# Performance work log

Hardware: AMD Instinct MI355X
Metric: run time of the kernel (lower is better)

Reference implementation:

```python
import jax, jax.numpy as jnp
import numpy as np

# Model dims (match init_kwargs / input_specs)
B, L, D = 4, 1024, 512
CHI, S = 32, 4          # bond_dim, spatial_bond_dim
TRUNC_THR = 1e-4        # relative SVD truncation threshold
LN_EPS = 1e-6


def setup_inputs() -> dict:
    key = jax.random.key(0)
    ks = jax.random.split(key, 6)
    def dense(k, fi, fo):
        return jax.random.normal(k, (fi, fo), jnp.float32) / np.float32(np.sqrt(fi))
    return {
        "x": jax.random.normal(ks[0], (B, L, D), jnp.float32),
        "W_site": dense(ks[1], D, CHI * S * CHI),
        "b_site": jnp.zeros((CHI * S * CHI,), jnp.float32),
        "W_bridge": dense(ks[2], S * CHI, CHI),
        "b_bridge": jnp.zeros((CHI,), jnp.float32),
        "W_out": dense(ks[3], CHI, D),
        "b_out": jnp.zeros((D,), jnp.float32),
        "gamma": jnp.ones((D,), jnp.float32),
        "beta": jnp.zeros((D,), jnp.float32),
        "W_gate": dense(ks[4], D, D),
        "b_gate": jnp.zeros((D,), jnp.float32),
    }


def _mps_temporal_scan(x, site_weights):
    """Sequential O(L*chi^2) MPS scan with per-step SVD truncation.

    x: [B, L, D]; site_weights: [B, L, chi, s, chi].
    State h_t [B, chi] is the (normalized) left environment vector. Each step
    contracts the left vector (state + input injection from the first chi
    features, since initial_state is zeros) with the site tensor, truncates
    small singular values (relative threshold), and accumulates log-norms.
    Returns outputs [B, L, s*chi] and log_probs [B, L].
    """
    u_seq = jnp.transpose(x[:, :, :CHI], (1, 0, 2))            # [L, B, chi]
    A_seq = jnp.transpose(site_weights, (1, 0, 2, 3, 4))        # [L, B, chi, s, chi]

    def step(h, inp):
        A, u = inp                                              # [B,chi,s,chi], [B,chi]
        left = h + u                                            # input-driven left vector
        M = jnp.einsum('bl,blpr->bpr', left, A)                 # [B, s, chi]
        U, Sv, Vh = jnp.linalg.svd(M, full_matrices=False)      # Sv: [B, min(s,chi)]
        mask = (Sv >= TRUNC_THR * Sv[:, :1]).astype(M.dtype)    # relative truncation
        St = Sv * mask
        Mt = jnp.einsum('bik,bk,bkr->bir', U, St, Vh)           # truncated site matrix
        nrm = jnp.sqrt(jnp.sum(St * St, axis=-1) + 1e-12)       # Frobenius norm -> log prob
        v = jnp.sum(Mt, axis=1)                                 # contract physical index
        h_new = v / (jnp.linalg.norm(v, axis=-1, keepdims=True) + 1e-12)
        return h_new, (Mt.reshape(Mt.shape[0], -1), jnp.log(nrm))

    h0 = jnp.zeros((x.shape[0], CHI), x.dtype)                  # initial_state = zeros
    _, (outs, logp) = jax.lax.scan(step, h0, (A_seq, u_seq))
    return jnp.transpose(outs, (1, 0, 2)), jnp.transpose(logp, (1, 0))


def reference(x, W_site, b_site, W_bridge, b_bridge, W_out, b_out,
              gamma, beta, W_gate, b_gate):
    x = x.astype(jnp.float32)
    Bb, Ll = x.shape[0], x.shape[1]
    # site_tensor_proj: Dense(chi*s*chi) applied directly to inputs
    site_weights = (x @ W_site + b_site).reshape(Bb, Ll, CHI, S, CHI)
    outs, _logp = _mps_temporal_scan(x, site_weights)           # [B, L, s*chi]
    y = outs @ W_bridge + b_bridge                              # mps_bridge -> [B,L,chi]
    y = y @ W_out + b_out                                       # output_projection -> [B,L,D]
    # LayerNorm(eps=1e-6)
    mu = jnp.mean(y, axis=-1, keepdims=True)
    var = jnp.mean((y - mu) ** 2, axis=-1, keepdims=True)
    yn = (y - mu) * jax.lax.rsqrt(var + LN_EPS) * gamma + beta
    # gated residual
    gate = jax.nn.sigmoid(x @ W_gate + b_gate)
    return gate * yn + (1.0 - gate) * x
```

## Files before the change

### kernel.cpp

```cpp
#include <hip/hip_runtime.h>
#include <math.h>

#define B_   4
#define L_   1024
#define D_   512
#define CHI_ 32
#define S_   4
#define BT_  (B_ * L_)
#define NC_  2560
#define DPRE 8

__device__ __forceinline__ float readlane_f(float v, int l) {
    return __int_as_float(__builtin_amdgcn_readlane(__float_as_int(v), l));
}

__device__ __forceinline__ float bpermute_f(int byte_idx, float v) {
    return __int_as_float(__builtin_amdgcn_ds_bpermute(byte_idx, __float_as_int(v)));
}

template <int CTRL>
__device__ __forceinline__ float dpp_add(float x) {
    int y = __builtin_amdgcn_update_dpp(0, __float_as_int(x), CTRL, 0xf, 0xf, true);
    return x + __int_as_float(y);
}

__device__ __forceinline__ float reduce32_to_lane31(float x) {
    x = dpp_add<0x111>(x);
    x = dpp_add<0x112>(x);
    x = dpp_add<0x114>(x);
    x = dpp_add<0x118>(x);
    x = dpp_add<0x142>(x);
    return x;
}

__device__ __forceinline__ float octet_sum(float x) {
    x = dpp_add<0x111>(x);
    x = dpp_add<0x112>(x);
    x = dpp_add<0x114>(x);
    return x;
}

__global__ __launch_bounds__(256) void buildW_kernel(
    const float* __restrict__ Ws, const float* __restrict__ bs,
    const float* __restrict__ Wb, const float* __restrict__ Wg,
    const float* __restrict__ bg, float* __restrict__ Wcomb,
    float* __restrict__ biasC)
{
    const int tid = threadIdx.x;

    if (blockIdx.x == 512) {
        for (int f = tid; f < NC_; f += 256) {
            float acc;
            if (f < 1024) {
                const int q = f >> 8, rem = f & 255, i = rem >> 2, e = rem & 3;
                const int l = 4 * (i & 7) + e, r = (i >> 3) + 8 * q;
                const float* p = bs + l * 128 + r;
                acc = p[0] + p[32] + p[64] + p[96];
            } else if (f < 2048) {
                const int g = f - 1024, l = g >> 5, j = g & 31;
                acc = 0.f;
                for (int pr = 0; pr < 128; ++pr)
                    acc = fmaf(bs[l * 128 + pr], Wb[pr * 32 + j], acc);
            } else {
                acc = bg[f - 2048];
            }
            biasC[f] = acc;
        }
        return;
    }

    __shared__ float wsrow[4096];
    __shared__ float wbs[4096];

    const int d = blockIdx.x;
    #pragma unroll
    for (int i = 0; i < 16; ++i) {
        wsrow[i * 256 + tid] = Ws[(size_t)d * 4096 + i * 256 + tid];
        wbs[i * 256 + tid]   = Wb[i * 256 + tid];
    }
    __syncthreads();

    float* wrow = Wcomb + (size_t)d * NC_;

    #pragma unroll
    for (int ii = 0; ii < 4; ++ii) {
        const int f = ii * 256 + tid;
        const int q = f >> 8, rem = f & 255, i = rem >> 2, e = rem & 3;
        const int l = 4 * (i & 7) + e, r = (i >> 3) + 8 * q;
        const float* p = wsrow + l * 128 + r;
        wrow[f] = p[0] + p[32] + p[64] + p[96];
    }
    #pragma unroll
    for (int ii = 0; ii < 4; ++ii) {
        const int g = ii * 256 + tid;
        const int l = g >> 5, j = g & 31;
        float acc = 0.f;
        #pragma unroll 8
        for (int pr = 0; pr < 128; ++pr)
            acc = fmaf(wsrow[l * 128 + pr], wbs[pr * 32 + j], acc);
        wrow[1024 + g] = acc;
    }
    #pragma unroll
    for (int ii = 0; ii < 2; ++ii) {
        const int c = ii * 256 + tid;
        wrow[2048 + c] = Wg[(size_t)d * 512 + c];
    }
}

__global__ __launch_bounds__(256) void gemm_bias_kernel(
    const float* __restrict__ A, const float* __restrict__ Bm,
    const float* __restrict__ bias, float* __restrict__ C,
    int M, int N, int K)
{
    __shared__ float As[32][68];
    __shared__ float Bs[32][64];

    const int tid = threadIdx.x;
    const int tx = tid & 15;
    const int ty = tid >> 4;
    const int m0 = blockIdx.y * 64;
    const int n0 = blockIdx.x * 64;

    float c[4][4] = {};

    for (int k0 = 0; k0 < K; k0 += 32) {
        {
            const int o = tid * 8;
            const int m = o >> 5;
            const int k = o & 31;
            const float* ap = A + (size_t)(m0 + m) * K + k0 + k;
            const float4 a0 = *(const float4*)ap;
            const float4 a1 = *(const float4*)(ap + 4);
            As[k + 0][m] = a0.x; As[k + 1][m] = a0.y;
            As[k + 2][m] = a0.z; As[k + 3][m] = a0.w;
            As[k + 4][m] = a1.x; As[k + 5][m] = a1.y;
            As[k + 6][m] = a1.z; As[k + 7][m] = a1.w;
        }
        {
            const int o = tid * 8;
            const int k = o >> 6;
            const int n = o & 63;
            const float* bp = Bm + (size_t)(k0 + k) * N + n0 + n;
            *(float4*)&Bs[k][n]     = *(const float4*)bp;
            *(float4*)&Bs[k][n + 4] = *(const float4*)(bp + 4);
        }
        __syncthreads();

        #pragma unroll
        for (int kk = 0; kk < 32; ++kk) {
            const float4 av = *(const float4*)&As[kk][ty * 4];
            const float4 bv = *(const float4*)&Bs[kk][tx * 4];
            const float a[4] = {av.x, av.y, av.z, av.w};
            const float b[4] = {bv.x, bv.y, bv.z, bv.w};
            #pragma unroll
            for (int i = 0; i < 4; ++i)
                #pragma unroll
                for (int j = 0; j < 4; ++j)
                    c[i][j] = fmaf(a[i], b[j], c[i][j]);
        }
        __syncthreads();
    }

    const float4 bv = *(const float4*)&bias[n0 + tx * 4];
    #pragma unroll
    for (int i = 0; i < 4; ++i) {
        float4 outv;
        outv.x = c[i][0] + bv.x;
        outv.y = c[i][1] + bv.y;
        outv.z = c[i][2] + bv.z;
        outv.w = c[i][3] + bv.w;
        *(float4*)&C[(size_t)(m0 + ty * 4 + i) * N + n0 + tx * 4] = outv;
    }
}

__global__ __launch_bounds__(256) void cvec_kernel(
    const float* __restrict__ Cc, const float* __restrict__ x,
    float* __restrict__ cBuf)
{
    const int tid  = threadIdx.x;
    const int lane = tid & 63;
    const int bt   = blockIdx.x * 4 + (tid >> 6);

    const float* base = Cc + (size_t)bt * NC_ + 4 * lane;
    float4 a0 = *(const float4*)(base + 0);
    float4 a1 = *(const float4*)(base + 256);
    float4 a2 = *(const float4*)(base + 512);
    float4 a3 = *(const float4*)(base + 768);

    const float u = x[(size_t)bt * D_ + (lane & 31)];
    const int idx0 = 16 * (lane & 7);
    const float u0 = bpermute_f(idx0 + 0,  u);
    const float u1 = bpermute_f(idx0 + 4,  u);
    const float u2 = bpermute_f(idx0 + 8,  u);
    const float u3 = bpermute_f(idx0 + 12, u);

    float p0 = fmaf(u3, a0.w, fmaf(u2, a0.z, fmaf(u1, a0.y, u0 * a0.x)));
    float p1 = fmaf(u3, a1.w, fmaf(u2, a1.z, fmaf(u1, a1.y, u0 * a1.x)));
    float p2 = fmaf(u3, a2.w, fmaf(u2, a2.z, fmaf(u1, a2.y, u0 * a2.x)));
    float p3 = fmaf(u3, a3.w, fmaf(u2, a3.z, fmaf(u1, a3.y, u0 * a3.x)));

    p0 = octet_sum(p0); p1 = octet_sum(p1);
    p2 = octet_sum(p2); p3 = octet_sum(p3);

    if ((lane & 7) == 7) {
        const int k = lane >> 3;
        float* cp = cBuf + (size_t)bt * 32 + k;
        cp[0]  = p0;
        cp[8]  = p1;
        cp[16] = p2;
        cp[24] = p3;
    }
}

__global__ __launch_bounds__(64, 1) void scan_kernel(
    const float* __restrict__ Cc, const float* __restrict__ cBuf,
    float* __restrict__ wOut)
{
    const int b   = blockIdx.x;
    const int tid = threadIdx.x;

    const float* At = Cc + (size_t)b * L_ * NC_ + 4 * tid;
    const float* cb = cBuf + (size_t)b * L_ * 32 + (tid & 31);
    float*       wo = wOut + (size_t)b * L_ * 64 + tid;

    const int idx0 = 16 * (tid & 7);
    const int idxR = 32 * (tid & 7) + 28;
    const bool selA = (tid >> 3) & 1;
    const bool selB = (tid >> 4) & 1;

    float4 areg[DPRE][4];
    float  creg[DPRE];

    #pragma unroll
    for (int j = 0; j < DPRE; ++j) {
        const float* ap = At + (size_t)j * NC_;
        #pragma unroll
        for (int q = 0; q < 4; ++q) areg[j][q] = *(const float4*)(ap + 256 * q);
        creg[j] = cb[j * 32];
    }

    float w = 0.f;

    for (int t = 0; t < L_; t += DPRE) {
        #pragma unroll
        for (int j = 0; j < DPRE; ++j) {
            wo[(t + j) * 64] = w;

            float red = reduce32_to_lane31(w * w);

            const float wb0 = bpermute_f(idx0 + 0,  w);
            const float wb1 = bpermute_f(idx0 + 4,  w);
            const float wb2 = bpermute_f(idx0 + 8,  w);
            const float wb3 = bpermute_f(idx0 + 12, w);

            float p0, p1, p2, p3;
            {
                const float4 a0 = areg[j][0], a1 = areg[j][1];
                const float4 a2 = areg[j][2], a3 = areg[j][3];
                p0 = fmaf(wb3, a0.w, fmaf(wb2, a0.z, fmaf(wb1, a0.y, wb0 * a0.x)));
                p1 = fmaf(wb3, a1.w, fmaf(wb2, a1.z, fmaf(wb1, a1.y, wb0 * a1.x)));
                p2 = fmaf(wb3, a2.w, fmaf(wb2, a2.z, fmaf(wb1, a2.y, wb0 * a2.x)));
                p3 = fmaf(wb3, a3.w, fmaf(wb2, a3.z, fmaf(wb1, a3.y, wb0 * a3.x)));
            }

            p0 = octet_sum(p0);
            p1 = octet_sum(p1);
            p2 = octet_sum(p2);
            p3 = octet_sum(p3);

            const float m0 = bpermute_f(idxR, p0);
            const float m1 = bpermute_f(idxR, p1);
            const float m2 = bpermute_f(idxR, p2);
            const float m3 = bpermute_f(idxR, p3);
            const float t0 = selA ? m1 : m0;
            const float t1 = selA ? m3 : m2;
            const float m  = selB ? t1 : t0;

            const float n2 = readlane_f(red, 31);
            const float rn = rsqrtf(n2 + 1e-24f);
            w = fmaf(m, rn, creg[j]);

            int tn = t + j + DPRE;
            if (tn > L_ - 1) tn = L_ - 1;
            const float* ap = At + (size_t)tn * NC_;
            #pragma unroll
            for (int q = 0; q < 4; ++q) areg[j][q] = *(const float4*)(ap + 256 * q);
            creg[j] = cb[tn * 32];
        }
    }
}

__global__ __launch_bounds__(128) void phaseB_kernel(
    const float* __restrict__ Cc, const float* __restrict__ x,
    const float* __restrict__ wBuf, const float* __restrict__ bb,
    float* __restrict__ y1)
{
    __shared__ float lf[32];
    __shared__ float part[4][32];

    const int bt = blockIdx.x;
    const int tid = threadIdx.x;

    if (tid < 64) {
        const float wv = wBuf[(size_t)bt * 64 + tid];
        float red = reduce32_to_lane31(wv * wv);
        const float n2 = readlane_f(red, 31);
        const float rn = rsqrtf(n2 + 1e-24f);
        if (tid < 32)
            lf[tid] = fmaf(wv, rn, x[(size_t)bt * D_ + tid]);
    }
    __syncthreads();

    const int j = tid & 31, q = tid >> 5;
    const float* Gp = Cc + (size_t)bt * NC_ + 1024;
    float p = 0.f;
    #pragma unroll
    for (int i = 0; i < 8; ++i)
        p = fmaf(lf[8 * q + i], Gp[(8 * q + i) * 32 + j], p);
    part[q][j] = p;
    __syncthreads();

    if (tid < 32)
        y1[bt * 32 + tid] = part[0][tid] + part[1][tid] + part[2][tid]
                          + part[3][tid] + bb[tid];
}

__global__ __launch_bounds__(256) void epilogue_kernel(
    const float* __restrict__ x, const float* __restrict__ y1buf,
    const float* __restrict__ Wout, const float* __restrict__ bout,
    const float* __restrict__ gamma, const float* __restrict__ beta,
    const float* __restrict__ Cc, float* __restrict__ out)
{
    __shared__ float ys[32];
    __shared__ float red1[4], red2[4];

    const int bt = blockIdx.x;
    const int tid = threadIdx.x;

    if (tid < 32) ys[tid] = y1buf[bt * 32 + tid];
    __syncthreads();

    float yv[2];
    #pragma unroll
    for (int q = 0; q < 2; ++q) {
        const int d = tid + q * 256;
        float acc = bout[d];
        #pragma unroll
        for (int j = 0; j < 32; ++j)
            acc = fmaf(ys[j], Wout[j * D_ + d], acc);
        yv[q] = acc;
    }

    float s1 = yv[0] + yv[1];
    float s2 = yv[0] * yv[0] + yv[1] * yv[1];
    #pragma unroll
    for (int m = 1; m <= 32; m <<= 1) {
        s1 += __shfl_xor(s1, m);
        s2 += __shfl_xor(s2, m);
    }
    const int wid = tid >> 6;
    if ((tid & 63) == 0) { red1[wid] = s1; red2[wid] = s2; }
    __syncthreads();
    const float S1 = red1[0] + red1[1] + red1[2] + red1[3];
    const float S2 = red2[0] + red2[1] + red2[2] + red2[3];
    const float mu  = S1 * (1.f / (float)D_);
    const float var = S2 * (1.f / (float)D_) - mu * mu;
    const float rstd = rsqrtf(var + 1e-6f);

    #pragma unroll
    for (int q = 0; q < 2; ++q) {
        const int d = tid + q * 256;
        const size_t gi = (size_t)bt * D_ + d;
        const float yn = (yv[q] - mu) * rstd * gamma[d] + beta[d];
        const float z = Cc[(size_t)bt * NC_ + 2048 + d];
        const float g = 1.f / (1.f + expf(-z));
        const float xv = x[gi];
        out[gi] = g * yn + (1.f - g) * xv;
    }
}

extern "C" void kernel_launch(void* const* d_in, const int* in_sizes, int n_in,
                              void* d_out, int out_size, void* d_ws, size_t ws_size,
                              hipStream_t stream)
{
    const float* x        = (const float*)d_in[0];
    const float* W_site   = (const float*)d_in[1];
    const float* b_site   = (const float*)d_in[2];
    const float* W_bridge = (const float*)d_in[3];
    const float* b_bridge = (const float*)d_in[4];
    const float* W_out    = (const float*)d_in[5];
    const float* b_out    = (const float*)d_in[6];
    const float* gamma    = (const float*)d_in[7];
    const float* beta     = (const float*)d_in[8];
    const float* W_gate   = (const float*)d_in[9];
    const float* b_gate   = (const float*)d_in[10];
    float* out = (float*)d_out;

    float* ws = (float*)d_ws;
    float* Wcomb = ws;
    float* biasC = Wcomb + (size_t)512 * NC_;
    float* Cc    = biasC + NC_;
    float* cBuf  = Cc    + (size_t)BT_ * NC_;
    float* wBuf  = cBuf  + (size_t)BT_ * 32;
    float* y1    = wBuf  + (size_t)BT_ * 64;

    buildW_kernel<<<dim3(513), dim3(256), 0, stream>>>(
        W_site, b_site, W_bridge, W_gate, b_gate, Wcomb, biasC);

    gemm_bias_kernel<<<dim3(NC_ / 64, BT_ / 64), dim3(256), 0, stream>>>(
        x, Wcomb, biasC, Cc, BT_, NC_, D_);

    cvec_kernel<<<dim3(BT_ / 4), dim3(256), 0, stream>>>(Cc, x, cBuf);

    scan_kernel<<<dim3(B_), dim3(64), 0, stream>>>(Cc, cBuf, wBuf);

    phaseB_kernel<<<dim3(BT_), dim3(128), 0, stream>>>(
        Cc, x, wBuf, b_bridge, y1);

    epilogue_kernel<<<dim3(BT_), dim3(256), 0, stream>>>(
        x, y1, W_out, b_out, gamma, beta, Cc, out);
}
```

Measured before the change: 461.7 us.

## Restructure scan to stream site tensors via global_load_lds ring buffer

The sequential scan kernel now prefetches each step's 1024-float site tensor and c-vector directly into a 16-slot LDS ring buffer using global_load_lds, with explicit vmcnt waits, instead of holding 8 steps of prefetched data in registers. The state is redistributed so each lane holds four components, computes the norm with an octet butterfly (no 32-lane reduction plus readlane), and writes the already-normalized state via raw buffer stores. The phaseB kernel therefore just reads the normalized state instead of recomputing the norm. This shortens the per-step dependency chain on the latency-bound single-wave scan, but relies on hand-tuned waitcnt counts and inline asm, which are fragile.

```diff
diff --git a/kernel.cpp b/kernel.cpp
--- a/kernel.cpp
+++ b/kernel.cpp
@@ -9,10 +9,8 @@
 #define BT_  (B_ * L_)
 #define NC_  2560
 #define DPRE 8
-
-__device__ __forceinline__ float readlane_f(float v, int l) {
-    return __int_as_float(__builtin_amdgcn_readlane(__float_as_int(v), l));
-}
+#define SLOTS 16
+#define SLOT_F 1088
 
 __device__ __forceinline__ float bpermute_f(int byte_idx, float v) {
     return __int_as_float(__builtin_amdgcn_ds_bpermute(byte_idx, __float_as_int(v)));
@@ -22,15 +20,6 @@
 __device__ __forceinline__ float dpp_add(float x) {
     int y = __builtin_amdgcn_update_dpp(0, __float_as_int(x), CTRL, 0xf, 0xf, true);
     return x + __int_as_float(y);
-}
-
-__device__ __forceinline__ float reduce32_to_lane31(float x) {
-    x = dpp_add<0x111>(x);
-    x = dpp_add<0x112>(x);
-    x = dpp_add<0x114>(x);
-    x = dpp_add<0x118>(x);
-    x = dpp_add<0x142>(x);
-    return x;
 }
 
 __device__ __forceinline__ float octet_sum(float x) {
@@ -38,6 +27,35 @@
     x = dpp_add<0x112>(x);
     x = dpp_add<0x114>(x);
     return x;
+}
+
+__device__ __forceinline__ float octet_bfly(float x) {
+    x = dpp_add<0xB1>(x);
+    x = dpp_add<0x4E>(x);
+    x = dpp_add<0x141>(x);
+    return x;
+}
+
+typedef __attribute__((ext_vector_type(4))) unsigned int srd_t;
+
+__device__ __forceinline__ srd_t make_srd(const void* p, unsigned bytes) {
+    const unsigned long long a = (unsigned long long)p;
+    srd_t r;
+    r.x = (unsigned)a;
+    r.y = (unsigned)(a >> 32);
+    r.z = bytes;
+    r.w = 0x00020000u;
+    return r;
+}
+
+typedef __attribute__((address_space(1))) const void gas1_void;
+typedef __attribute__((address_space(3))) void las3_void;
+
+__device__ __forceinline__ void gl_lds16(const float* g, float* l) {
+    __builtin_amdgcn_global_load_lds((gas1_void*)g, (las3_void*)l, 16, 0, 0);
+}
+__device__ __forceinline__ void gl_lds4(const float* g, float* l) {
+    __builtin_amdgcn_global_load_lds((gas1_void*)g, (las3_void*)l, 4, 0, 0);
 }
 
 __global__ __launch_bounds__(256) void buildW_kernel(
@@ -212,87 +230,135 @@
     }
 }
 
+#define SCAN_STEP(TT, W)                                                        \
+    do {                                                                        \
+        const int t_is = (TT) + DPRE;                                           \
+        {                                                                       \
+            float* sl = ldsb + (t_is & (SLOTS - 1)) * SLOT_F;                   \
+            const float* ar = Abase + (size_t)t_is * NC_ + 4 * tid;             \
+            gl_lds16(ar,       sl);                                             \
+            gl_lds16(ar + 256, sl + 256);                                       \
+            gl_lds16(ar + 512, sl + 512);                                       \
+            gl_lds16(ar + 768, sl + 768);                                       \
+            gl_lds4(cbase + (size_t)t_is * 32 + tid, sl + 1024);                \
+        }                                                                       \
+        __builtin_amdgcn_sched_barrier(0);                                      \
+        asm volatile("s_waitcnt vmcnt(" W ")");                                 \
+        __builtin_amdgcn_sched_barrier(0);                                      \
+        const float* sr = ldsb + (((TT) + 1) & (SLOTS - 1)) * SLOT_F;           \
+        const float4 nA0 = *(const float4*)(sr + 4 * tid);                      \
+        const float4 nA1 = *(const float4*)(sr + 256 + 4 * tid);                \
+        const float4 nA2 = *(const float4*)(sr + 512 + 4 * tid);                \
+        const float4 nA3 = *(const float4*)(sr + 768 + 4 * tid);                \
+        const float4 nC  = *(const float4*)(sr + 1024 + 4 * h);                 \
+        float nn = fmaf(wb1, wb1, wb0 * wb0)                                    \
+                 + fmaf(wb3, wb3, wb2 * wb2);                                   \
+        nn = octet_bfly(nn);                                                    \
+        const float rn = rsqrtf(nn + 1e-24f);                                   \
+        float p0 = fmaf(wb1, cA0.y, wb0 * cA0.x)                                \
+                 + fmaf(wb3, cA0.w, wb2 * cA0.z);                               \
+        float p1 = fmaf(wb1, cA1.y, wb0 * cA1.x)                                \
+                 + fmaf(wb3, cA1.w, wb2 * cA1.z);                               \
+        float p2 = fmaf(wb1, cA2.y, wb0 * cA2.x)                                \
+                 + fmaf(wb3, cA2.w, wb2 * cA2.z);                               \
+        float p3 = fmaf(wb1, cA3.y, wb0 * cA3.x)                                \
+                 + fmaf(wb3, cA3.w, wb2 * cA3.z);                               \
+        p0 = octet_bfly(p0);                                                    \
+        p1 = octet_bfly(p1);                                                    \
+        p2 = octet_bfly(p2);                                                    \
+        p3 = octet_bfly(p3);                                                    \
+        const float rp = (tid & 2) ? ((tid & 1) ? p3 : p2)                      \
+                                   : ((tid & 1) ? p1 : p0);                     \
+        const float m0 = bpermute_f(idx0,      rp);                             \
+        const float m1 = bpermute_f(idx0 + 32, rp);                             \
+        const float m2 = bpermute_f(idx0 + 64, rp);                             \
+        const float m3 = bpermute_f(idx0 + 96, rp);                             \
+        const unsigned long long s01 =                                          \
+            ((unsigned long long)__float_as_uint(wb1 * rn) << 32) |             \
+            (unsigned)__float_as_uint(wb0 * rn);                                \
+        const unsigned long long s23 =                                          \
+            ((unsigned long long)__float_as_uint(wb3 * rn) << 32) |             \
+            (unsigned)__float_as_uint(wb2 * rn);                                \
+        asm volatile("buffer_store_dwordx2 %1, %0, %2, 0 offen"                 \
+                     :: "v"(voffW), "v"(s01), "s"(srdW));                       \
+        asm volatile("buffer_store_dwordx2 %1, %0, %2, 0 offen offset:8"        \
+                     :: "v"(voffW), "v"(s23), "s"(srdW));                       \
+        voffW += 128u;                                                          \
+        wb0 = fmaf(m0, rn, cC.x);                                               \
+        wb1 = fmaf(m1, rn, cC.y);                                               \
+        wb2 = fmaf(m2, rn, cC.z);                                               \
+        wb3 = fmaf(m3, rn, cC.w);                                               \
+        cA0 = nA0; cA1 = nA1; cA2 = nA2; cA3 = nA3; cC = nC;                    \
+        __builtin_amdgcn_sched_barrier(0);                                      \
+    } while (0)
+
 __global__ __launch_bounds__(64, 1) void scan_kernel(
     const float* __restrict__ Cc, const float* __restrict__ cBuf,
-    float* __restrict__ wOut)
-{
+    float* __restrict__ hnOut)
+{
+    __shared__ __align__(16) float ldsb[SLOTS * SLOT_F];
+
     const int b   = blockIdx.x;
     const int tid = threadIdx.x;
-
-    const float* At = Cc + (size_t)b * L_ * NC_ + 4 * tid;
-    const float* cb = cBuf + (size_t)b * L_ * 32 + (tid & 31);
-    float*       wo = wOut + (size_t)b * L_ * 64 + tid;
-
-    const int idx0 = 16 * (tid & 7);
-    const int idxR = 32 * (tid & 7) + 28;
-    const bool selA = (tid >> 3) & 1;
-    const bool selB = (tid >> 4) & 1;
-
-    float4 areg[DPRE][4];
-    float  creg[DPRE];
+    const int h   = tid & 7;
+
+    const float* Abase = Cc   + (size_t)b * L_ * NC_;
+    const float* cbase = cBuf + (size_t)b * L_ * 32;
+    const srd_t  srdW  = make_srd(hnOut + (size_t)b * L_ * 32,
+                                  (unsigned)(L_ * 32 * 4));
+
+    const int idx0 = 4 * (32 * (h & 1) + (h >> 1));
+
+    unsigned voffW = (unsigned)(h * 16);
 
     #pragma unroll
     for (int j = 0; j < DPRE; ++j) {
-        const float* ap = At + (size_t)j * NC_;
-        #pragma unroll
-        for (int q = 0; q < 4; ++q) areg[j][q] = *(const float4*)(ap + 256 * q);
-        creg[j] = cb[j * 32];
-    }
-
-    float w = 0.f;
-
-    for (int t = 0; t < L_; t += DPRE) {
-        #pragma unroll
-        for (int j = 0; j < DPRE; ++j) {
-            wo[(t + j) * 64] = w;
-
-            float red = reduce32_to_lane31(w * w);
-
-            const float wb0 = bpermute_f(idx0 + 0,  w);
-            const float wb1 = bpermute_f(idx0 + 4,  w);
-            const float wb2 = bpermute_f(idx0 + 8,  w);
-            const float wb3 = bpermute_f(idx0 + 12, w);
-
-            float p0, p1, p2, p3;
-            {
-                const float4 a0 = areg[j][0], a1 = areg[j][1];
-                const float4 a2 = areg[j][2], a3 = areg[j][3];
-                p0 = fmaf(wb3, a0.w, fmaf(wb2, a0.z, fmaf(wb1, a0.y, wb0 * a0.x)));
-                p1 = fmaf(wb3, a1.w, fmaf(wb2, a1.z, fmaf(wb1, a1.y, wb0 * a1.x)));
-                p2 = fmaf(wb3, a2.w, fmaf(wb2, a2.z, fmaf(wb1, a2.y, wb0 * a2.x)));
-                p3 = fmaf(wb3, a3.w, fmaf(wb2, a3.z, fmaf(wb1, a3.y, wb0 * a3.x)));
-            }
-
-            p0 = octet_sum(p0);
-            p1 = octet_sum(p1);
-            p2 = octet_sum(p2);
-            p3 = octet_sum(p3);
-
-            const float m0 = bpermute_f(idxR, p0);
-            const float m1 = bpermute_f(idxR, p1);
-            const float m2 = bpermute_f(idxR, p2);
-            const float m3 = bpermute_f(idxR, p3);
-            const float t0 = selA ? m1 : m0;
-            const float t1 = selA ? m3 : m2;
-            const float m  = selB ? t1 : t0;
-
-            const float n2 = readlane_f(red, 31);
-            const float rn = rsqrtf(n2 + 1e-24f);
-            w = fmaf(m, rn, creg[j]);
-
-            int tn = t + j + DPRE;
-            if (tn > L_ - 1) tn = L_ - 1;
-            const float* ap = At + (size_t)tn * NC_;
-            #pragma unroll
-            for (int q = 0; q < 4; ++q) areg[j][q] = *(const float4*)(ap + 256 * q);
-            creg[j] = cb[tn * 32];
-        }
-    }
-}
+        float* sl = ldsb + j * SLOT_F;
+        const float* ar = Abase + (size_t)j * NC_ + 4 * tid;
+        gl_lds16(ar,       sl);
+        gl_lds16(ar + 256, sl + 256);
+        gl_lds16(ar + 512, sl + 512);
+        gl_lds16(ar + 768, sl + 768);
+        gl_lds4(cbase + (size_t)j * 32 + tid, sl + 1024);
+    }
+    __builtin_amdgcn_sched_barrier(0);
+    asm volatile("s_waitcnt vmcnt(35)");
+    __builtin_amdgcn_sched_barrier(0);
+
+    float4 cA0 = *(const float4*)(ldsb + 4 * tid);
+    float4 cA1 = *(const float4*)(ldsb + 256 + 4 * tid);
+    float4 cA2 = *(const float4*)(ldsb + 512 + 4 * tid);
+    float4 cA3 = *(const float4*)(ldsb + 768 + 4 * tid);
+    float4 cC  = *(const float4*)(ldsb + 1024 + 4 * h);
+
+    float wb0 = 0.f, wb1 = 0.f, wb2 = 0.f, wb3 = 0.f;
+
+    SCAN_STEP(0, "35");
+    SCAN_STEP(1, "37");
+    SCAN_STEP(2, "39");
+    SCAN_STEP(3, "41");
+    SCAN_STEP(4, "43");
+    SCAN_STEP(5, "45");
+    SCAN_STEP(6, "47");
+    SCAN_STEP(7, "49");
+
+    for (int t = DPRE; t < L_; t += DPRE) {
+        SCAN_STEP(t + 0, "49");
+        SCAN_STEP(t + 1, "49");
+        SCAN_STEP(t + 2, "49");
+        SCAN_STEP(t + 3, "49");
+        SCAN_STEP(t + 4, "49");
+        SCAN_STEP(t + 5, "49");
+        SCAN_STEP(t + 6, "49");
+        SCAN_STEP(t + 7, "49");
+    }
+    asm volatile("s_waitcnt vmcnt(0)");
+}
+#undef SCAN_STEP
 
 __global__ __launch_bounds__(128) void phaseB_kernel(
     const float* __restrict__ Cc, const float* __restrict__ x,
-    const float* __restrict__ wBuf, const float* __restrict__ bb,
+    const float* __restrict__ hnBuf, const float* __restrict__ bb,
     float* __restrict__ y1)
 {
     __shared__ float lf[32];
@@ -301,14 +367,8 @@
     const int bt = blockIdx.x;
     const int tid = threadIdx.x;
 
-    if (tid < 64) {
-        const float wv = wBuf[(size_t)bt * 64 + tid];
-        float red = reduce32_to_lane31(wv * wv);
-        const float n2 = readlane_f(red, 31);
-        const float rn = rsqrtf(n2 + 1e-24f);
-        if (tid < 32)
-            lf[tid] = fmaf(wv, rn, x[(size_t)bt * D_ + tid]);
-    }
+    if (tid < 32)
+        lf[tid] = hnBuf[(size_t)bt * 32 + tid] + x[(size_t)bt * D_ + tid];
     __syncthreads();
 
     const int j = tid & 31, q = tid >> 5;
@@ -401,8 +461,8 @@
     float* biasC = Wcomb + (size_t)512 * NC_;
     float* Cc    = biasC + NC_;
     float* cBuf  = Cc    + (size_t)BT_ * NC_;
-    float* wBuf  = cBuf  + (size_t)BT_ * 32;
-    float* y1    = wBuf  + (size_t)BT_ * 64;
+    float* hnBuf = cBuf  + (size_t)BT_ * 32;
+    float* y1    = hnBuf + (size_t)BT_ * 32;
 
     buildW_kernel<<<dim3(513), dim3(256), 0, stream>>>(
         W_site, b_site, W_bridge, W_gate, b_gate, Wcomb, biasC);
@@ -412,10 +472,10 @@
 
     cvec_kernel<<<dim3(BT_ / 4), dim3(256), 0, stream>>>(Cc, x, cBuf);
 
-    scan_kernel<<<dim3(B_), dim3(64), 0, stream>>>(Cc, cBuf, wBuf);
+    scan_kernel<<<dim3(B_), dim3(64), 0, stream>>>(Cc, cBuf, hnBuf);
 
     phaseB_kernel<<<dim3(BT_), dim3(128), 0, stream>>>(
-        Cc, x, wBuf, b_bridge, y1);
+        Cc, x, hnBuf, b_bridge, y1);
 
     epilogue_kernel<<<dim3(BT_), dim3(256), 0, stream>>>(
         x, y1, W_out, b_out, gamma, beta, Cc, out);
```

Result: slower. 642.0 us (+39.1%).

## Enlarge GEMM tile to 128x128 with 8x8 register micro-tiles per thread

Applied to the files above, without the earlier changes.

The fp32 GEMM that produces the combined site/bridge/gate projections now uses 128x128 block tiles, with each thread computing an 8x8 register tile instead of 4x4. This doubles arithmetic per shared-memory load and cuts global reloads of A and B tiles. In exchange it raises register pressure and leaves only 20x32=640 blocks, which could lower occupancy on a 256-CU device.

```diff
diff --git a/kernel.cpp b/kernel.cpp
--- a/kernel.cpp
+++ b/kernel.cpp
@@ -112,34 +112,32 @@
     const float* __restrict__ bias, float* __restrict__ C,
     int M, int N, int K)
 {
-    __shared__ float As[32][68];
-    __shared__ float Bs[32][64];
+    __shared__ float As[32][132];
+    __shared__ float Bs[32][132];
 
     const int tid = threadIdx.x;
     const int tx = tid & 15;
     const int ty = tid >> 4;
-    const int m0 = blockIdx.y * 64;
-    const int n0 = blockIdx.x * 64;
-
-    float c[4][4] = {};
+    const int m0 = blockIdx.y * 128;
+    const int n0 = blockIdx.x * 128;
+
+    float acc[8][8] = {};
 
     for (int k0 = 0; k0 < K; k0 += 32) {
-        {
-            const int o = tid * 8;
-            const int m = o >> 5;
-            const int k = o & 31;
-            const float* ap = A + (size_t)(m0 + m) * K + k0 + k;
-            const float4 a0 = *(const float4*)ap;
-            const float4 a1 = *(const float4*)(ap + 4);
-            As[k + 0][m] = a0.x; As[k + 1][m] = a0.y;
-            As[k + 2][m] = a0.z; As[k + 3][m] = a0.w;
-            As[k + 4][m] = a1.x; As[k + 5][m] = a1.y;
-            As[k + 6][m] = a1.z; As[k + 7][m] = a1.w;
+        #pragma unroll
+        for (int p = 0; p < 4; ++p) {
+            const int m = (tid >> 3) + 32 * p;
+            const int k = (tid & 7) * 4;
+            const float4 av = *(const float4*)(A + (size_t)(m0 + m) * K + k0 + k);
+            As[k + 0][m] = av.x;
+            As[k + 1][m] = av.y;
+            As[k + 2][m] = av.z;
+            As[k + 3][m] = av.w;
         }
-        {
-            const int o = tid * 8;
-            const int k = o >> 6;
-            const int n = o & 63;
+        #pragma unroll
+        for (int p = 0; p < 2; ++p) {
+            const int k = (tid >> 4) + 16 * p;
+            const int n = (tid & 15) * 8;
             const float* bp = Bm + (size_t)(k0 + k) * N + n0 + n;
             *(float4*)&Bs[k][n]     = *(const float4*)bp;
             *(float4*)&Bs[k][n + 4] = *(const float4*)(bp + 4);
@@ -148,28 +146,33 @@
 
         #pragma unroll
         for (int kk = 0; kk < 32; ++kk) {
-            const float4 av = *(const float4*)&As[kk][ty * 4];
-            const float4 bv = *(const float4*)&Bs[kk][tx * 4];
-            const float a[4] = {av.x, av.y, av.z, av.w};
-            const float b[4] = {bv.x, bv.y, bv.z, bv.w};
+            const float4 a0 = *(const float4*)&As[kk][ty * 8];
+            const float4 a1 = *(const float4*)&As[kk][ty * 8 + 4];
+            const float4 b0 = *(const float4*)&Bs[kk][tx * 8];
+            const float4 b1 = *(const float4*)&Bs[kk][tx * 8 + 4];
+            const float a[8] = {a0.x, a0.y, a0.z, a0.w, a1.x, a1.y, a1.z, a1.w};
+            const float b[8] = {b0.x, b0.y, b0.z, b0.w, b1.x, b1.y, b1.z, b1.w};
             #pragma unroll
-            for (int i = 0; i < 4; ++i)
+            for (int i = 0; i < 8; ++i)
                 #pragma unroll
-                for (int j = 0; j < 4; ++j)
-                    c[i][j] = fmaf(a[i], b[j], c[i][j]);
+                for (int j = 0; j < 8; ++j)
+                    acc[i][j] = fmaf(a[i], b[j], acc[i][j]);
         }
         __syncthreads();
     }
 
-    const float4 bv = *(const float4*)&bias[n0 + tx * 4];
-    #pragma unroll
-    for (int i = 0; i < 4; ++i) {
-        float4 outv;
-        outv.x = c[i][0] + bv.x;
-        outv.y = c[i][1] + bv.y;
-        outv.z = c[i][2] + bv.z;
-        outv.w = c[i][3] + bv.w;
-        *(float4*)&C[(size_t)(m0 + ty * 4 + i) * N + n0 + tx * 4] = outv;
+    const float4 bv0 = *(const float4*)&bias[n0 + tx * 8];
+    const float4 bv1 = *(const float4*)&bias[n0 + tx * 8 + 4];
+    #pragma unroll
+    for (int i = 0; i < 8; ++i) {
+        float* cp = C + (size_t)(m0 + ty * 8 + i) * N + n0 + tx * 8;
+        float4 o0, o1;
+        o0.x = acc[i][0] + bv0.x; o0.y = acc[i][1] + bv0.y;
+        o0.z = acc[i][2] + bv0.z; o0.w = acc[i][3] + bv0.w;
+        o1.x = acc[i][4] + bv1.x; o1.y = acc[i][5] + bv1.y;
+        o1.z = acc[i][6] + bv1.z; o1.w = acc[i][7] + bv1.w;
+        *(float4*)cp       = o0;
+        *(float4*)(cp + 4) = o1;
     }
 }
 
@@ -407,7 +410,7 @@
     buildW_kernel<<<dim3(513), dim3(256), 0, stream>>>(
         W_site, b_site, W_bridge, W_gate, b_gate, Wcomb, biasC);
 
-    gemm_bias_kernel<<<dim3(NC_ / 64, BT_ / 64), dim3(256), 0, stream>>>(
+    gemm_bias_kernel<<<dim3(NC_ / 128, BT_ / 128), dim3(256), 0, stream>>>(
         x, Wcomb, biasC, Cc, BT_, NC_, D_);
 
     cvec_kernel<<<dim3(BT_ / 4), dim3(256), 0, stream>>>(Cc, x, cBuf);
```

New measurement: 455.0 us. Within noise of the previous version (-1.5%).
